# Performance work log

Hardware: AMD Instinct MI355X
Metric: run time of the kernel (lower is better)

## Reference

```python
import jax, jax.numpy as jnp
import numpy as np

IN_FEATURES = 1024
OUT_FEATURES = 1024
THRESHOLD = 0.05


def ternary_quantize(x, threshold):
    # {-1, 0, +1}: zero where |x| < threshold, else sign(x)
    return jnp.where(jnp.abs(x) < threshold, jnp.zeros_like(x), jnp.sign(x))


def setup_inputs() -> dict:
    key = jax.random.key(0)
    kx, kw = jax.random.split(key)
    x = jax.random.normal(kx, (32768, IN_FEATURES), dtype=jnp.float32)
    # xavier_uniform for weight [out, in]: bound = sqrt(6/(fan_in+fan_out))
    bound = float(np.sqrt(6.0 / (IN_FEATURES + OUT_FEATURES)))
    weight = jax.random.uniform(kw, (OUT_FEATURES, IN_FEATURES), dtype=jnp.float32,
                                minval=-bound, maxval=bound)
    return {"x": x, "weight": weight}


def reference(x, weight):
    x_tern = ternary_quantize(x, THRESHOLD).astype(jnp.int8)
    w_tern = ternary_quantize(weight, THRESHOLD).astype(jnp.int8)
    # int32 accumulate matmul: [T, in] @ [in, out] -> [T, out]
    out = jnp.matmul(x_tern.astype(jnp.int32), w_tern.astype(jnp.int32).T)
    return out.astype(jnp.float32)
```

## Files before the change

### kernel.cpp

```cpp
#include <hip/hip_runtime.h>

#define THRESH 0.05f

typedef __attribute__((ext_vector_type(4))) int int32x4;

__global__ __launch_bounds__(256) void quant_w_kernel(const float* __restrict__ w,
                                                      signed char* __restrict__ wqf) {
    int c = blockIdx.x * 256 + threadIdx.x;
    int l15  = c & 15;
    int quad = (c >> 4) & 3;
    int nb   = (c >> 6) & 63;
    int kb   = c >> 12;
    int col   = nb * 16 + l15;
    int kbase = kb * 64 + quad * 16;
    const float* src = w + col * 1024 + kbase;
    signed char q[16];
    #pragma unroll
    for (int j = 0; j < 4; ++j) {
        float4 f = *(const float4*)(src + j * 4);
        q[j * 4 + 0] = (signed char)((f.x >= THRESH) - (f.x <= -THRESH));
        q[j * 4 + 1] = (signed char)((f.y >= THRESH) - (f.y <= -THRESH));
        q[j * 4 + 2] = (signed char)((f.z >= THRESH) - (f.z <= -THRESH));
        q[j * 4 + 3] = (signed char)((f.w >= THRESH) - (f.w <= -THRESH));
    }
    *(int32x4*)(wqf + (size_t)c * 16) = *(const int32x4*)q;
}

__global__ __launch_bounds__(256, 4) void tern_gemm_kernel(const float* __restrict__ x,
                                                           const signed char* __restrict__ wqf,
                                                           float* __restrict__ out) {
    __shared__ __attribute__((aligned(16))) signed char a_lds[32 * 1024];
    const int tid = threadIdx.x;
    const long rowbase = (long)blockIdx.x * 32;

    #pragma unroll
    for (int i = 0; i < 8; ++i) {
        int c   = tid + i * 256;
        int row = c >> 6;
        int cir = c & 63;
        const float4* src = (const float4*)(x + (rowbase + row) * 1024 + cir * 16);
        signed char q[16];
        #pragma unroll
        for (int j = 0; j < 4; ++j) {
            float4 f = src[j];
            q[j * 4 + 0] = (signed char)((f.x >= THRESH) - (f.x <= -THRESH));
            q[j * 4 + 1] = (signed char)((f.y >= THRESH) - (f.y <= -THRESH));
            q[j * 4 + 2] = (signed char)((f.z >= THRESH) - (f.z <= -THRESH));
            q[j * 4 + 3] = (signed char)((f.w >= THRESH) - (f.w <= -THRESH));
        }
        int swz = (cir ^ (row & 7)) * 16;
        *(int32x4*)(a_lds + row * 1024 + swz) = *(const int32x4*)q;
    }
    __syncthreads();

    const int wave = tid >> 6;
    const int lane = tid & 63;
    const int l15  = lane & 15;
    const int lq   = lane >> 4;

    for (int ct = 0; ct < 4; ++ct) {
        const int cb = wave * 256 + ct * 64;
        const int nb_base = cb >> 4;
        int32x4 acc[2][4];
        #pragma unroll
        for (int ri = 0; ri < 2; ++ri)
            #pragma unroll
            for (int ci = 0; ci < 4; ++ci)
                acc[ri][ci] = (int32x4){0, 0, 0, 0};

        for (int k = 0; k < 16; ++k) {
            const int kchunk = k * 4 + lq;

            int32x4 afrag[2];
            #pragma unroll
            for (int ri = 0; ri < 2; ++ri) {
                int m = ri * 16 + l15;
                afrag[ri] = *(const int32x4*)(a_lds + m * 1024 + ((kchunk ^ (m & 7)) * 16));
            }

            int32x4 bfrag[4];
            #pragma unroll
            for (int ci = 0; ci < 4; ++ci) {
                bfrag[ci] = *(const int32x4*)(wqf + (size_t)(k * 64 + nb_base + ci) * 1024 + lane * 16);
            }

            #pragma unroll
            for (int ri = 0; ri < 2; ++ri)
                #pragma unroll
                for (int ci = 0; ci < 4; ++ci)
                    acc[ri][ci] = __builtin_amdgcn_mfma_i32_16x16x64_i8(
                        bfrag[ci], afrag[ri], acc[ri][ci], 0, 0, 0);
        }

        #pragma unroll
        for (int ri = 0; ri < 2; ++ri) {
            const long row = rowbase + ri * 16 + l15;
            #pragma unroll
            for (int ci = 0; ci < 4; ++ci) {
                float4 v;
                v.x = (float)acc[ri][ci][0];
                v.y = (float)acc[ri][ci][1];
                v.z = (float)acc[ri][ci][2];
                v.w = (float)acc[ri][ci][3];
                const int col = cb + ci * 16 + lq * 4;
                *(float4*)(out + row * 1024 + col) = v;
            }
        }
    }
}

extern "C" void kernel_launch(void* const* d_in, const int* in_sizes, int n_in,
                              void* d_out, int out_size, void* d_ws, size_t ws_size,
                              hipStream_t stream) {
    const float* x = (const float*)d_in[0];
    const float* w = (const float*)d_in[1];
    float* out = (float*)d_out;
    signed char* wqf = (signed char*)d_ws;

    quant_w_kernel<<<dim3(256), dim3(256), 0, stream>>>(w, wqf);
    tern_gemm_kernel<<<dim3(1024), dim3(256), 0, stream>>>(x, wqf, out);
}
```

Measured before the change: 329.8 us.

## Restructure GEMM loop to prefetch full B column strip and use nontemporal IO

Each wave now processes one 16-column block per iteration across 16 iterations. All 16 K-step B fragments are loaded into registers up front behind a sched barrier, so global loads are batched and their latency is exposed once per strip rather than once per K step. The x reads and output writes use nontemporal load and store to avoid polluting the cache. In exchange, each A fragment is reused across only one column block instead of four, which raises LDS traffic, and the 16 B registers per lane add register pressure.

After: 288.1 us. -12.6%, faster.

```diff
diff --git a/kernel.cpp b/kernel.cpp
--- a/kernel.cpp
+++ b/kernel.cpp
@@ -2,7 +2,8 @@
 
 #define THRESH 0.05f
 
-typedef __attribute__((ext_vector_type(4))) int int32x4;
+typedef __attribute__((ext_vector_type(4))) int   int32x4;
+typedef __attribute__((ext_vector_type(4))) float floatx4;
 
 __global__ __launch_bounds__(256) void quant_w_kernel(const float* __restrict__ w,
                                                       signed char* __restrict__ wqf) {
@@ -38,15 +39,14 @@
         int c   = tid + i * 256;
         int row = c >> 6;
         int cir = c & 63;
-        const float4* src = (const float4*)(x + (rowbase + row) * 1024 + cir * 16);
+        const floatx4* src = (const floatx4*)(x + (rowbase + row) * 1024 + cir * 16);
         signed char q[16];
         #pragma unroll
         for (int j = 0; j < 4; ++j) {
-            float4 f = src[j];
-            q[j * 4 + 0] = (signed char)((f.x >= THRESH) - (f.x <= -THRESH));
-            q[j * 4 + 1] = (signed char)((f.y >= THRESH) - (f.y <= -THRESH));
-            q[j * 4 + 2] = (signed char)((f.z >= THRESH) - (f.z <= -THRESH));
-            q[j * 4 + 3] = (signed char)((f.w >= THRESH) - (f.w <= -THRESH));
+            floatx4 f = __builtin_nontemporal_load(src + j);
+            #pragma unroll
+            for (int e = 0; e < 4; ++e)
+                q[j * 4 + e] = (signed char)((f[e] >= THRESH) - (f[e] <= -THRESH));
         }
         int swz = (cir ^ (row & 7)) * 16;
         *(int32x4*)(a_lds + row * 1024 + swz) = *(const int32x4*)q;
@@ -58,53 +58,40 @@
     const int l15  = lane & 15;
     const int lq   = lane >> 4;
 
-    for (int ct = 0; ct < 4; ++ct) {
-        const int cb = wave * 256 + ct * 64;
-        const int nb_base = cb >> 4;
-        int32x4 acc[2][4];
+    for (int colit = 0; colit < 16; ++colit) {
+        const int nb = colit * 4 + wave;
+
+        int32x4 bf[16];
         #pragma unroll
-        for (int ri = 0; ri < 2; ++ri)
-            #pragma unroll
-            for (int ci = 0; ci < 4; ++ci)
-                acc[ri][ci] = (int32x4){0, 0, 0, 0};
+        for (int k = 0; k < 16; ++k)
+            bf[k] = *(const int32x4*)(wqf + (size_t)(k * 64 + nb) * 1024 + lane * 16);
+        __builtin_amdgcn_sched_barrier(0);
 
+        int32x4 acc[2];
+        acc[0] = (int32x4){0, 0, 0, 0};
+        acc[1] = (int32x4){0, 0, 0, 0};
+
+        #pragma unroll
         for (int k = 0; k < 16; ++k) {
             const int kchunk = k * 4 + lq;
-
-            int32x4 afrag[2];
             #pragma unroll
             for (int ri = 0; ri < 2; ++ri) {
                 int m = ri * 16 + l15;
-                afrag[ri] = *(const int32x4*)(a_lds + m * 1024 + ((kchunk ^ (m & 7)) * 16));
+                int32x4 af = *(const int32x4*)(a_lds + m * 1024 + ((kchunk ^ (m & 7)) * 16));
+                acc[ri] = __builtin_amdgcn_mfma_i32_16x16x64_i8(bf[k], af, acc[ri], 0, 0, 0);
             }
-
-            int32x4 bfrag[4];
-            #pragma unroll
-            for (int ci = 0; ci < 4; ++ci) {
-                bfrag[ci] = *(const int32x4*)(wqf + (size_t)(k * 64 + nb_base + ci) * 1024 + lane * 16);
-            }
-
-            #pragma unroll
-            for (int ri = 0; ri < 2; ++ri)
-                #pragma unroll
-                for (int ci = 0; ci < 4; ++ci)
-                    acc[ri][ci] = __builtin_amdgcn_mfma_i32_16x16x64_i8(
-                        bfrag[ci], afrag[ri], acc[ri][ci], 0, 0, 0);
         }
 
+        const int cb = colit * 64 + wave * 16;
         #pragma unroll
         for (int ri = 0; ri < 2; ++ri) {
             const long row = rowbase + ri * 16 + l15;
-            #pragma unroll
-            for (int ci = 0; ci < 4; ++ci) {
-                float4 v;
-                v.x = (float)acc[ri][ci][0];
-                v.y = (float)acc[ri][ci][1];
-                v.z = (float)acc[ri][ci][2];
-                v.w = (float)acc[ri][ci][3];
-                const int col = cb + ci * 16 + lq * 4;
-                *(float4*)(out + row * 1024 + col) = v;
-            }
+            floatx4 v;
+            v[0] = (float)acc[ri][0];
+            v[1] = (float)acc[ri][1];
+            v[2] = (float)acc[ri][2];
+            v[3] = (float)acc[ri][3];
+            __builtin_nontemporal_store(v, (floatx4*)(out + row * 1024 + cb + lq * 4));
         }
     }
 }
```
